# Optimization experiments

Hardware: AMD Instinct MI355X
Metric: run time of the kernel (lower is better)

The kernel has to match this reference:

```python
import jax, jax.numpy as jnp
import numpy as np

H = 64
N = 200000
E = 2000000
EPS = 1e-5


def layernorm(x, g, b):
    mu = jnp.mean(x, axis=-1, keepdims=True)
    var = jnp.var(x, axis=-1, keepdims=True)
    return (x - mu) * jax.lax.rsqrt(var + EPS) * g + b


def setup_inputs() -> dict:
    key = jax.random.key(0)
    ks = jax.random.split(key, 12)
    s = 0.02
    return {
        "z": jax.random.normal(ks[0], (N, H), dtype=jnp.float32),
        "pot_arcs": jax.random.randint(ks[1], (E, 2), 0, N + 1, dtype=jnp.int64),
        "root_w": jax.random.normal(ks[2], (H, 1), dtype=jnp.float32) * s,
        "root_b": jax.random.normal(ks[3], (H,), dtype=jnp.float32) * s,
        "lin1_w": jax.random.normal(ks[4], (H, H), dtype=jnp.float32) * s,
        "lin1_b": jax.random.normal(ks[5], (H,), dtype=jnp.float32) * s,
        "lin2_w": jax.random.normal(ks[6], (H, H), dtype=jnp.float32) * s,
        "lin2_b": jax.random.normal(ks[7], (H,), dtype=jnp.float32) * s,
        "bil_w": jax.random.normal(ks[8], (1, H, H), dtype=jnp.float32) * s,
        "bil_b": jax.random.normal(ks[9], (1,), dtype=jnp.float32) * s,
        "norm_g": jnp.ones((H,), dtype=jnp.float32),
        "norm_b": jnp.zeros((H,), dtype=jnp.float32),
    }


def reference(z, pot_arcs, root_w, root_b, lin1_w, lin1_b, lin2_w, lin2_b,
              bil_w, bil_b, norm_g, norm_b):
    # root feature: Linear(1->H) applied to ones((1,1)) => root_w[:,0] + root_b
    root_feat = (root_w[:, 0] + root_b)[None, :]           # [1, H]
    zz = jnp.concatenate([root_feat, z], axis=0)           # [N+1, H]
    zz = layernorm(zz, norm_g, norm_b)

    # edge gather (irregular access)
    h1 = zz[pot_arcs[:, 0]]                                # [E, H]
    h2 = zz[pot_arcs[:, 1]]                                # [E, H]

    # dual linear -> relu -> LayerNorm (dropout = identity in eval)
    x1 = layernorm(jax.nn.relu(h1 @ lin1_w.T + lin1_b), norm_g, norm_b)
    x2 = layernorm(jax.nn.relu(h2 @ lin2_w.T + lin2_b), norm_g, norm_b)

    # bilinear score: x1 @ W[0] @ x2 per edge, +b
    score = jnp.einsum('eh,hg,eg->e', x1, bil_w[0], x2) + bil_b[0]
    return score                                            # [E]
```

## Files before the change

kernel.cpp:

```cpp
#include <hip/hip_runtime.h>
#include <hip/hip_bf16.h>

typedef unsigned short u16;
typedef unsigned int u32;

typedef float f32x4 __attribute__((ext_vector_type(4)));
typedef short bf16x8 __attribute__((ext_vector_type(8)));

#define HDIM 64
#define EPS 1e-5f
#define XROW 68


__device__ __forceinline__ float wave_sum64(float v) {
    v += __shfl_xor(v, 1, 64);
    v += __shfl_xor(v, 2, 64);
    v += __shfl_xor(v, 4, 64);
    v += __shfl_xor(v, 8, 64);
    v += __shfl_xor(v, 16, 64);
    v += __shfl_xor(v, 32, 64);
    return v;
}

__device__ __forceinline__ float bcast(float v, int k) {
    return __int_as_float(__builtin_amdgcn_readlane(__float_as_int(v), k));
}

__device__ __forceinline__ u16 f2bf(float f) {
    u32 u = __float_as_uint(f);
    u32 r = (u + 0x7fffu + ((u >> 16) & 1u)) >> 16;
    return (u16)r;
}

__device__ __forceinline__ float bflo(u32 w) { return __uint_as_float(w << 16); }
__device__ __forceinline__ float bfhi(u32 w) { return __uint_as_float(w & 0xffff0000u); }

__global__ __launch_bounds__(256) void prep_kernel(
    const float* __restrict__ lin1_w, const float* __restrict__ lin2_w,
    const float* __restrict__ bil_w,
    u16* __restrict__ w1bf, u16* __restrict__ w2bf, u16* __restrict__ btbf)
{
    const int tid = threadIdx.x;
    for (int i = tid; i < 4096; i += 256) {
        w1bf[i] = f2bf(lin1_w[i]);
        w2bf[i] = f2bf(lin2_w[i]);
        const int g = i >> 6, h = i & 63;
        btbf[i] = f2bf(bil_w[h * 64 + g]);
    }
}

__device__ __forceinline__ bf16x8 load_afrag(const u16* Xs, int l, int m, int s) {
    const int row = 16 * m + (l & 15);
    const int k0  = 8 * (l >> 4) + 32 * s;
    union { uint2 u[2]; bf16x8 f; } c;
    c.u[0] = *(const uint2*)&Xs[row * XROW + k0];
    c.u[1] = *(const uint2*)&Xs[row * XROW + k0 + 4];
    return c.f;
}

__device__ __forceinline__ bf16x8 load_bfrag(const u16* __restrict__ W,
                                             int l, int t, int s) {
    const int n  = (l & 15) + 16 * t;
    const int k0 = 8 * (l >> 4) + 32 * s;
    return *(const bf16x8*)&W[n * 64 + k0];
}

__device__ __forceinline__ void relu_ln_acc(f32x4* acc, const float* biasv,
                                            const float* gv, const float* bvv) {
    float s[4] = {0.f,0.f,0.f,0.f}, q[4] = {0.f,0.f,0.f,0.f};
#pragma unroll
    for (int t = 0; t < 4; ++t)
#pragma unroll
        for (int j = 0; j < 4; ++j) {
            float v = fmaxf(acc[t][j] + biasv[t], 0.f);
            acc[t][j] = v;
            s[j] += v; q[j] = fmaf(v, v, q[j]);
        }
#pragma unroll
    for (int j = 0; j < 4; ++j) {
#pragma unroll
        for (int m = 1; m < 16; m <<= 1) {
            s[j] += __shfl_xor(s[j], m, 64);
            q[j] += __shfl_xor(q[j], m, 64);
        }
        const float mu = s[j] * 0.015625f;
        const float rs = rsqrtf(q[j] * 0.015625f - mu * mu + EPS);
#pragma unroll
        for (int t = 0; t < 4; ++t)
            acc[t][j] = (acc[t][j] - mu) * rs * gv[t] + bvv[t];
    }
}

__device__ __forceinline__ void acc_to_lds(u16* Xs, const f32x4* acc, int l, int m) {
    const int hcol = l & 15;
#pragma unroll
    for (int j = 0; j < 4; ++j) {
        const int row = 16 * m + (l >> 4) * 4 + j;
#pragma unroll
        for (int t = 0; t < 4; ++t)
            Xs[row * XROW + hcol + 16 * t] = f2bf(acc[t][j]);
    }
}

__device__ __forceinline__ void lds_to_global32(u16* __restrict__ T, const u16* Xs,
                                                int l, int n0, int nnodes) {
    const int row  = l >> 1;
    const int node = n0 + row;
    if (node >= nnodes) return;
    const int c0 = (l & 1) * 32;
    const u16* src = &Xs[row * XROW + c0];
    uint2 p[8];
#pragma unroll
    for (int j = 0; j < 8; ++j) p[j] = *(const uint2*)&src[4*j];
    uint4* d = (uint4*)(T + (size_t)node * HDIM + c0);
    d[0] = make_uint4(p[0].x, p[0].y, p[1].x, p[1].y);
    d[1] = make_uint4(p[2].x, p[2].y, p[3].x, p[3].y);
    d[2] = make_uint4(p[4].x, p[4].y, p[5].x, p[5].y);
    d[3] = make_uint4(p[6].x, p[6].y, p[7].x, p[7].y);
}

__global__ __launch_bounds__(256) void phase1_kernel(
    const float* __restrict__ z,
    const float* __restrict__ root_w, const float* __restrict__ root_b,
    const u16* __restrict__ w1bf, const float* __restrict__ lin1_b,
    const u16* __restrict__ w2bf, const float* __restrict__ lin2_b,
    const u16* __restrict__ btbf,
    const float* __restrict__ norm_g, const float* __restrict__ norm_b,
    u16* __restrict__ T1, u16* __restrict__ T2, int nnodes)
{
    __shared__ u16 XsAll[4][32 * XROW];

    const int tid = threadIdx.x;
    const int wid = tid >> 6;
    const int l   = tid & 63;
    u16* Xs = XsAll[wid];

    const int n0 = (blockIdx.x * 4 + wid) * 32;

    {
        const int row  = l >> 1;
        const int node = n0 + row;
        const int c0   = (l & 1) * 32;
        float r[32];
        if (node == 0) {
#pragma unroll
            for (int qq = 0; qq < 8; ++qq) {
                const float4 a = *(const float4*)&root_w[c0 + 4*qq];
                const float4 b = *(const float4*)&root_b[c0 + 4*qq];
                r[4*qq] = a.x + b.x; r[4*qq+1] = a.y + b.y;
                r[4*qq+2] = a.z + b.z; r[4*qq+3] = a.w + b.w;
            }
        } else if (node < nnodes) {
            const float4* zp = (const float4*)(z + (size_t)(node - 1) * HDIM + c0);
#pragma unroll
            for (int qq = 0; qq < 8; ++qq) {
                const float4 v = zp[qq];
                r[4*qq] = v.x; r[4*qq+1] = v.y; r[4*qq+2] = v.z; r[4*qq+3] = v.w;
            }
        } else {
#pragma unroll
            for (int k = 0; k < 32; ++k) r[k] = 0.f;
        }
        float s = 0.f, sq = 0.f;
#pragma unroll
        for (int k = 0; k < 32; ++k) { s += r[k]; sq = fmaf(r[k], r[k], sq); }
        s  += __shfl_xor(s, 1, 64);  sq += __shfl_xor(sq, 1, 64);
        const float mu = s * 0.015625f;
        const float rs = rsqrtf(sq * 0.015625f - mu * mu + EPS);
        u16* dst = &Xs[row * XROW + c0];
#pragma unroll
        for (int qq = 0; qq < 8; ++qq) {
            const float4 g4 = *(const float4*)&norm_g[c0 + 4*qq];
            const float4 b4 = *(const float4*)&norm_b[c0 + 4*qq];
            u16 t0 = f2bf((r[4*qq]   - mu) * rs * g4.x + b4.x);
            u16 t1 = f2bf((r[4*qq+1] - mu) * rs * g4.y + b4.y);
            u16 t2 = f2bf((r[4*qq+2] - mu) * rs * g4.z + b4.z);
            u16 t3 = f2bf((r[4*qq+3] - mu) * rs * g4.w + b4.w);
            uint2 pw;
            pw.x = (u32)t0 | ((u32)t1 << 16);
            pw.y = (u32)t2 | ((u32)t3 << 16);
            *(uint2*)&dst[4*qq] = pw;
        }
    }

    const int hcol = l & 15;
    float gv[4], bv[4], b1v[4], b2v[4];
#pragma unroll
    for (int t = 0; t < 4; ++t) {
        gv[t]  = norm_g[hcol + 16*t];
        bv[t]  = norm_b[hcol + 16*t];
        b1v[t] = lin1_b[hcol + 16*t];
        b2v[t] = lin2_b[hcol + 16*t];
    }

    bf16x8 a[2][2];
#pragma unroll
    for (int m = 0; m < 2; ++m) {
        a[m][0] = load_afrag(Xs, l, m, 0);
        a[m][1] = load_afrag(Xs, l, m, 1);
    }

    f32x4 acc2[2][4], acc1[2][4];
#pragma unroll
    for (int t = 0; t < 4; ++t) {
        const bf16x8 b0 = load_bfrag(w2bf, l, t, 0);
        const bf16x8 b1 = load_bfrag(w2bf, l, t, 1);
#pragma unroll
        for (int m = 0; m < 2; ++m) {
            f32x4 c = {0.f, 0.f, 0.f, 0.f};
            c = __builtin_amdgcn_mfma_f32_16x16x32_bf16(a[m][0], b0, c, 0, 0, 0);
            c = __builtin_amdgcn_mfma_f32_16x16x32_bf16(a[m][1], b1, c, 0, 0, 0);
            acc2[m][t] = c;
        }
    }
#pragma unroll
    for (int t = 0; t < 4; ++t) {
        const bf16x8 b0 = load_bfrag(w1bf, l, t, 0);
        const bf16x8 b1 = load_bfrag(w1bf, l, t, 1);
#pragma unroll
        for (int m = 0; m < 2; ++m) {
            f32x4 c = {0.f, 0.f, 0.f, 0.f};
            c = __builtin_amdgcn_mfma_f32_16x16x32_bf16(a[m][0], b0, c, 0, 0, 0);
            c = __builtin_amdgcn_mfma_f32_16x16x32_bf16(a[m][1], b1, c, 0, 0, 0);
            acc1[m][t] = c;
        }
    }

    relu_ln_acc(acc2[0], b2v, gv, bv);
    relu_ln_acc(acc2[1], b2v, gv, bv);
    acc_to_lds(Xs, acc2[0], l, 0);
    acc_to_lds(Xs, acc2[1], l, 1);
    lds_to_global32(T2, Xs, l, n0, nnodes);

    relu_ln_acc(acc1[0], b1v, gv, bv);
    relu_ln_acc(acc1[1], b1v, gv, bv);
    acc_to_lds(Xs, acc1[0], l, 0);
    acc_to_lds(Xs, acc1[1], l, 1);
#pragma unroll
    for (int m = 0; m < 2; ++m) {
        a[m][0] = load_afrag(Xs, l, m, 0);
        a[m][1] = load_afrag(Xs, l, m, 1);
    }

    f32x4 acc3[2][4];
#pragma unroll
    for (int t = 0; t < 4; ++t) {
        const bf16x8 b0 = load_bfrag(btbf, l, t, 0);
        const bf16x8 b1 = load_bfrag(btbf, l, t, 1);
#pragma unroll
        for (int m = 0; m < 2; ++m) {
            f32x4 c = {0.f, 0.f, 0.f, 0.f};
            c = __builtin_amdgcn_mfma_f32_16x16x32_bf16(a[m][0], b0, c, 0, 0, 0);
            c = __builtin_amdgcn_mfma_f32_16x16x32_bf16(a[m][1], b1, c, 0, 0, 0);
            acc3[m][t] = c;
        }
    }
    acc_to_lds(Xs, acc3[0], l, 0);
    acc_to_lds(Xs, acc3[1], l, 1);
    lds_to_global32(T1, Xs, l, n0, nnodes);
}

__device__ __forceinline__ float dot8(uint4 u, uint4 v) {
    float s = 0.f;
    s = fmaf(bflo(u.x), bflo(v.x), s); s = fmaf(bfhi(u.x), bfhi(v.x), s);
    s = fmaf(bflo(u.y), bflo(v.y), s); s = fmaf(bfhi(u.y), bfhi(v.y), s);
    s = fmaf(bflo(u.z), bflo(v.z), s); s = fmaf(bfhi(u.z), bfhi(v.z), s);
    s = fmaf(bflo(u.w), bflo(v.w), s); s = fmaf(bfhi(u.w), bfhi(v.w), s);
    return s;
}

__global__ __launch_bounds__(256) void phase2_kernel(
    const int* __restrict__ arcs,
    const u16* __restrict__ T1, const u16* __restrict__ T2,
    const float* __restrict__ bil_b,
    float* __restrict__ out, int E)
{
    const int gtid = blockIdx.x * 256 + threadIdx.x;
    const int wv = gtid >> 6;
    const int l  = gtid & 63;
    const int l8 = l & 7;
    const int le = l >> 3;
    const int e0 = wv * 16 + le;
    const int e1 = e0 + 8;
    const bool ok0 = e0 < E, ok1 = e1 < E;

    uint4 u0, v0, u1, v1;
    if (ok0) {
        const int i0 = arcs[2 * e0], j0 = arcs[2 * e0 + 1];
        u0 = *((const uint4*)(T1 + (size_t)i0 * HDIM) + l8);
        v0 = *((const uint4*)(T2 + (size_t)j0 * HDIM) + l8);
    }
    if (ok1) {
        const int i1 = arcs[2 * e1], j1 = arcs[2 * e1 + 1];
        u1 = *((const uint4*)(T1 + (size_t)i1 * HDIM) + l8);
        v1 = *((const uint4*)(T2 + (size_t)j1 * HDIM) + l8);
    }

    float s0 = ok0 ? dot8(u0, v0) : 0.f;
    float s1 = ok1 ? dot8(u1, v1) : 0.f;

    s0 += __shfl_xor(s0, 1, 64);  s1 += __shfl_xor(s1, 1, 64);
    s0 += __shfl_xor(s0, 2, 64);  s1 += __shfl_xor(s1, 2, 64);
    s0 += __shfl_xor(s0, 4, 64);  s1 += __shfl_xor(s1, 4, 64);

    if (l8 == 0) {
        const float bb = bil_b[0];
        if (ok0) __builtin_nontemporal_store(s0 + bb, &out[e0]);
        if (ok1) __builtin_nontemporal_store(s1 + bb, &out[e1]);
    }
}

__device__ __forceinline__ float lnorm_w(float v, float g, float b) {
    float mu = wave_sum64(v) * 0.015625f;
    float d  = v - mu;
    float var = wave_sum64(d * d) * 0.015625f;
    return d * rsqrtf(var + EPS) * g + b;
}

__global__ __launch_bounds__(256) void edge_direct_kernel(
    const float* __restrict__ z, const int* __restrict__ arcs,
    const float* __restrict__ root_w, const float* __restrict__ root_b,
    const float* __restrict__ lin1_w, const float* __restrict__ lin1_b,
    const float* __restrict__ lin2_w, const float* __restrict__ lin2_b,
    const float* __restrict__ bil_w, const float* __restrict__ bil_b,
    const float* __restrict__ norm_g, const float* __restrict__ norm_b,
    float* __restrict__ out, int E, int nnodes)
{
    __shared__ float W1t[4096], W2t[4096], Bs[4096];
    const int tid = threadIdx.x;
    for (int i = tid; i < 4096; i += 256) {
        int h = i >> 6, k = i & 63;
        W1t[(k << 6) | h] = lin1_w[i];
        W2t[(k << 6) | h] = lin2_w[i];
        Bs[i] = bil_w[i];
    }
    __syncthreads();

    const int lane = tid & 63;
    const float g  = norm_g[lane], bt = norm_b[lane];
    const float b1 = lin1_b[lane], b2 = lin2_b[lane];
    const float rootv = root_w[lane] + root_b[lane];

    const int gwave = (blockIdx.x * 256 + tid) >> 6;
    const int nwaves = (gridDim.x * 256) >> 6;

    for (int e = gwave; e < E; e += nwaves) {
        int i0 = arcs[2 * e], i1 = arcs[2 * e + 1];
        float v0 = (i0 == 0) ? rootv : z[(size_t)(i0 - 1) * HDIM + lane];
        float v1 = (i1 == 0) ? rootv : z[(size_t)(i1 - 1) * HDIM + lane];
        float l0 = lnorm_w(v0, g, bt);
        float l1 = lnorm_w(v1, g, bt);
        float a1 = 0.f, a2 = 0.f;
#pragma unroll
        for (int k = 0; k < 64; ++k) {
            a1 = fmaf(bcast(l0, k), W1t[(k << 6) | lane], a1);
            a2 = fmaf(bcast(l1, k), W2t[(k << 6) | lane], a2);
        }
        float x1 = lnorm_w(fmaxf(a1 + b1, 0.f), g, bt);
        float x2 = lnorm_w(fmaxf(a2 + b2, 0.f), g, bt);
        float w1 = 0.f;
#pragma unroll
        for (int h = 0; h < 64; ++h)
            w1 = fmaf(bcast(x1, h), Bs[(h << 6) | lane], w1);
        float sc = wave_sum64(w1 * x2);
        if (lane == 0) out[e] = sc + bil_b[0];
    }
}

extern "C" void kernel_launch(void* const* d_in, const int* in_sizes, int n_in,
                              void* d_out, int out_size, void* d_ws, size_t ws_size,
                              hipStream_t stream) {
    const float* z      = (const float*)d_in[0];
    const int*   arcs   = (const int*)  d_in[1];
    const float* root_w = (const float*)d_in[2];
    const float* root_b = (const float*)d_in[3];
    const float* lin1_w = (const float*)d_in[4];
    const float* lin1_b = (const float*)d_in[5];
    const float* lin2_w = (const float*)d_in[6];
    const float* lin2_b = (const float*)d_in[7];
    const float* bil_w  = (const float*)d_in[8];
    const float* bil_b  = (const float*)d_in[9];
    const float* norm_g = (const float*)d_in[10];
    const float* norm_b = (const float*)d_in[11];
    float* out = (float*)d_out;

    const int E      = in_sizes[1] / 2;
    const int nnodes = in_sizes[0] / HDIM + 1;

    const size_t tbl  = (size_t)nnodes * HDIM * sizeof(u16);
    const size_t need = 2 * tbl + 3 * 4096 * sizeof(u16);

    if (ws_size >= need) {
        u16* T1   = (u16*)d_ws;
        u16* T2   = (u16*)((char*)d_ws + tbl);
        u16* w1bf = (u16*)((char*)d_ws + 2 * tbl);
        u16* w2bf = w1bf + 4096;
        u16* btbf = w2bf + 4096;

        prep_kernel<<<1, 256, 0, stream>>>(lin1_w, lin2_w, bil_w, w1bf, w2bf, btbf);

        const int blocks1 = (nnodes + 127) / 128;
        phase1_kernel<<<blocks1, 256, 0, stream>>>(
            z, root_w, root_b, w1bf, lin1_b, w2bf, lin2_b, btbf,
            norm_g, norm_b, T1, T2, nnodes);

        const long long thr2 = (long long)E * 4;
        const int blocks2 = (int)((thr2 + 255) / 256);
        phase2_kernel<<<blocks2, 256, 0, stream>>>(arcs, T1, T2, bil_b, out, E);
    } else {
        edge_direct_kernel<<<8192, 256, 0, stream>>>(
            z, arcs, root_w, root_b, lin1_w, lin1_b, lin2_w, lin2_b,
            bil_w, bil_b, norm_g, norm_b, out, E, nnodes);
    }
}
```

Before: 132.6 us.

## Build MFMA A-fragments in registers, simplify edge gather, widen prep grid

Phase 1 now has each lane load and layer-normalize exactly the row slices it needs for its MFMA A-fragments. This skips the LDS write/read round trip, and the row statistics are reduced across lanes with shuffles. Phase 2 is rewritten to handle one edge per 8 threads instead of two edges per 8 lanes, which doubles the thread count and drops the nontemporal stores. The weight prep kernel now runs on 16 blocks instead of 1. Together these aim to cut LDS traffic and serial prep time, but phase 2 launches more threads and does less work per thread, which may hurt gather latency hiding.

```diff
diff --git a/kernel.cpp b/kernel.cpp
--- a/kernel.cpp
+++ b/kernel.cpp
@@ -32,6 +32,9 @@
     return (u16)r;
 }
 
+__device__ __forceinline__ u32 pack2(float e0, float e1) {
+    return (u32)f2bf(e0) | ((u32)f2bf(e1) << 16);
+}
 __device__ __forceinline__ float bflo(u32 w) { return __uint_as_float(w << 16); }
 __device__ __forceinline__ float bfhi(u32 w) { return __uint_as_float(w & 0xffff0000u); }
 
@@ -40,8 +43,8 @@
     const float* __restrict__ bil_w,
     u16* __restrict__ w1bf, u16* __restrict__ w2bf, u16* __restrict__ btbf)
 {
-    const int tid = threadIdx.x;
-    for (int i = tid; i < 4096; i += 256) {
+    const int gtid = blockIdx.x * 256 + threadIdx.x;
+    for (int i = gtid; i < 4096; i += gridDim.x * 256) {
         w1bf[i] = f2bf(lin1_w[i]);
         w2bf[i] = f2bf(lin2_w[i]);
         const int g = i >> 6, h = i & 63;
@@ -137,50 +140,71 @@
 
     const int n0 = (blockIdx.x * 4 + wid) * 32;
 
-    {
-        const int row  = l >> 1;
-        const int node = n0 + row;
-        const int c0   = (l & 1) * 32;
-        float r[32];
+    const int arow = l & 15;
+    const int kg   = (l >> 4) * 8;
+
+    float4 gk0 = *(const float4*)&norm_g[kg];
+    float4 gk1 = *(const float4*)&norm_g[kg + 4];
+    float4 gk2 = *(const float4*)&norm_g[kg + 32];
+    float4 gk3 = *(const float4*)&norm_g[kg + 36];
+    float4 bk0 = *(const float4*)&norm_b[kg];
+    float4 bk1 = *(const float4*)&norm_b[kg + 4];
+    float4 bk2 = *(const float4*)&norm_b[kg + 32];
+    float4 bk3 = *(const float4*)&norm_b[kg + 36];
+
+    bf16x8 a[2][2];
+#pragma unroll
+    for (int m = 0; m < 2; ++m) {
+        const int node = n0 + 16 * m + arow;
+        float r[16];
         if (node == 0) {
 #pragma unroll
-            for (int qq = 0; qq < 8; ++qq) {
-                const float4 a = *(const float4*)&root_w[c0 + 4*qq];
-                const float4 b = *(const float4*)&root_b[c0 + 4*qq];
-                r[4*qq] = a.x + b.x; r[4*qq+1] = a.y + b.y;
-                r[4*qq+2] = a.z + b.z; r[4*qq+3] = a.w + b.w;
+            for (int q = 0; q < 2; ++q) {
+                const float4 aw = *(const float4*)&root_w[kg + 4*q];
+                const float4 ab = *(const float4*)&root_b[kg + 4*q];
+                r[4*q]   = aw.x + ab.x; r[4*q+1] = aw.y + ab.y;
+                r[4*q+2] = aw.z + ab.z; r[4*q+3] = aw.w + ab.w;
+                const float4 cw = *(const float4*)&root_w[kg + 32 + 4*q];
+                const float4 cb = *(const float4*)&root_b[kg + 32 + 4*q];
+                r[8+4*q]   = cw.x + cb.x; r[8+4*q+1] = cw.y + cb.y;
+                r[8+4*q+2] = cw.z + cb.z; r[8+4*q+3] = cw.w + cb.w;
             }
         } else if (node < nnodes) {
-            const float4* zp = (const float4*)(z + (size_t)(node - 1) * HDIM + c0);
-#pragma unroll
-            for (int qq = 0; qq < 8; ++qq) {
-                const float4 v = zp[qq];
-                r[4*qq] = v.x; r[4*qq+1] = v.y; r[4*qq+2] = v.z; r[4*qq+3] = v.w;
-            }
+            const float* zp = z + (size_t)(node - 1) * HDIM + kg;
+            const float4 v0 = *(const float4*)(zp);
+            const float4 v1 = *(const float4*)(zp + 4);
+            const float4 v2 = *(const float4*)(zp + 32);
+            const float4 v3 = *(const float4*)(zp + 36);
+            r[0]=v0.x; r[1]=v0.y; r[2]=v0.z; r[3]=v0.w;
+            r[4]=v1.x; r[5]=v1.y; r[6]=v1.z; r[7]=v1.w;
+            r[8]=v2.x; r[9]=v2.y; r[10]=v2.z; r[11]=v2.w;
+            r[12]=v3.x; r[13]=v3.y; r[14]=v3.z; r[15]=v3.w;
         } else {
 #pragma unroll
-            for (int k = 0; k < 32; ++k) r[k] = 0.f;
+            for (int k = 0; k < 16; ++k) r[k] = 0.f;
         }
         float s = 0.f, sq = 0.f;
 #pragma unroll
-        for (int k = 0; k < 32; ++k) { s += r[k]; sq = fmaf(r[k], r[k], sq); }
-        s  += __shfl_xor(s, 1, 64);  sq += __shfl_xor(sq, 1, 64);
+        for (int k = 0; k < 16; ++k) { s += r[k]; sq = fmaf(r[k], r[k], sq); }
+        s += __shfl_xor(s, 16, 64);  sq += __shfl_xor(sq, 16, 64);
+        s += __shfl_xor(s, 32, 64);  sq += __shfl_xor(sq, 32, 64);
         const float mu = s * 0.015625f;
         const float rs = rsqrtf(sq * 0.015625f - mu * mu + EPS);
-        u16* dst = &Xs[row * XROW + c0];
-#pragma unroll
-        for (int qq = 0; qq < 8; ++qq) {
-            const float4 g4 = *(const float4*)&norm_g[c0 + 4*qq];
-            const float4 b4 = *(const float4*)&norm_b[c0 + 4*qq];
-            u16 t0 = f2bf((r[4*qq]   - mu) * rs * g4.x + b4.x);
-            u16 t1 = f2bf((r[4*qq+1] - mu) * rs * g4.y + b4.y);
-            u16 t2 = f2bf((r[4*qq+2] - mu) * rs * g4.z + b4.z);
-            u16 t3 = f2bf((r[4*qq+3] - mu) * rs * g4.w + b4.w);
-            uint2 pw;
-            pw.x = (u32)t0 | ((u32)t1 << 16);
-            pw.y = (u32)t2 | ((u32)t3 << 16);
-            *(uint2*)&dst[4*qq] = pw;
-        }
+
+        const float gA[8] = {gk0.x,gk0.y,gk0.z,gk0.w, gk1.x,gk1.y,gk1.z,gk1.w};
+        const float bA[8] = {bk0.x,bk0.y,bk0.z,bk0.w, bk1.x,bk1.y,bk1.z,bk1.w};
+        const float gB[8] = {gk2.x,gk2.y,gk2.z,gk2.w, gk3.x,gk3.y,gk3.z,gk3.w};
+        const float bB[8] = {bk2.x,bk2.y,bk2.z,bk2.w, bk3.x,bk3.y,bk3.z,bk3.w};
+        union { u32 u[4]; bf16x8 f; } c0, c1;
+#pragma unroll
+        for (int j = 0; j < 4; ++j) {
+            c0.u[j] = pack2((r[2*j]   - mu) * rs * gA[2*j]   + bA[2*j],
+                            (r[2*j+1] - mu) * rs * gA[2*j+1] + bA[2*j+1]);
+            c1.u[j] = pack2((r[8+2*j]   - mu) * rs * gB[2*j]   + bB[2*j],
+                            (r[8+2*j+1] - mu) * rs * gB[2*j+1] + bB[2*j+1]);
+        }
+        a[m][0] = c0.f;
+        a[m][1] = c1.f;
     }
 
     const int hcol = l & 15;
@@ -193,13 +217,6 @@
         b2v[t] = lin2_b[hcol + 16*t];
     }
 
-    bf16x8 a[2][2];
-#pragma unroll
-    for (int m = 0; m < 2; ++m) {
-        a[m][0] = load_afrag(Xs, l, m, 0);
-        a[m][1] = load_afrag(Xs, l, m, 1);
-    }
-
     f32x4 acc2[2][4], acc1[2][4];
 #pragma unroll
     for (int t = 0; t < 4; ++t) {
@@ -258,15 +275,6 @@
     acc_to_lds(Xs, acc3[0], l, 0);
     acc_to_lds(Xs, acc3[1], l, 1);
     lds_to_global32(T1, Xs, l, n0, nnodes);
-}
-
-__device__ __forceinline__ float dot8(uint4 u, uint4 v) {
-    float s = 0.f;
-    s = fmaf(bflo(u.x), bflo(v.x), s); s = fmaf(bfhi(u.x), bfhi(v.x), s);
-    s = fmaf(bflo(u.y), bflo(v.y), s); s = fmaf(bfhi(u.y), bfhi(v.y), s);
-    s = fmaf(bflo(u.z), bflo(v.z), s); s = fmaf(bfhi(u.z), bfhi(v.z), s);
-    s = fmaf(bflo(u.w), bflo(v.w), s); s = fmaf(bfhi(u.w), bfhi(v.w), s);
-    return s;
 }
 
 __global__ __launch_bounds__(256) void phase2_kernel(
@@ -275,39 +283,33 @@
     const float* __restrict__ bil_b,
     float* __restrict__ out, int E)
 {
-    const int gtid = blockIdx.x * 256 + threadIdx.x;
-    const int wv = gtid >> 6;
-    const int l  = gtid & 63;
-    const int l8 = l & 7;
-    const int le = l >> 3;
-    const int e0 = wv * 16 + le;
-    const int e1 = e0 + 8;
-    const bool ok0 = e0 < E, ok1 = e1 < E;
-
-    uint4 u0, v0, u1, v1;
-    if (ok0) {
-        const int i0 = arcs[2 * e0], j0 = arcs[2 * e0 + 1];
-        u0 = *((const uint4*)(T1 + (size_t)i0 * HDIM) + l8);
-        v0 = *((const uint4*)(T2 + (size_t)j0 * HDIM) + l8);
-    }
-    if (ok1) {
-        const int i1 = arcs[2 * e1], j1 = arcs[2 * e1 + 1];
-        u1 = *((const uint4*)(T1 + (size_t)i1 * HDIM) + l8);
-        v1 = *((const uint4*)(T2 + (size_t)j1 * HDIM) + l8);
-    }
-
-    float s0 = ok0 ? dot8(u0, v0) : 0.f;
-    float s1 = ok1 ? dot8(u1, v1) : 0.f;
-
-    s0 += __shfl_xor(s0, 1, 64);  s1 += __shfl_xor(s1, 1, 64);
-    s0 += __shfl_xor(s0, 2, 64);  s1 += __shfl_xor(s1, 2, 64);
-    s0 += __shfl_xor(s0, 4, 64);  s1 += __shfl_xor(s1, 4, 64);
-
-    if (l8 == 0) {
-        const float bb = bil_b[0];
-        if (ok0) __builtin_nontemporal_store(s0 + bb, &out[e0]);
-        if (ok1) __builtin_nontemporal_store(s1 + bb, &out[e1]);
-    }
+    const int tid = blockIdx.x * 256 + threadIdx.x;
+    const int e = tid >> 3;
+    if (e >= E) return;
+    const int l8 = tid & 7;
+
+    const int i0 = arcs[2 * e];
+    const int i1 = arcs[2 * e + 1];
+
+    const uint4* p1 = (const uint4*)(T1 + (size_t)i0 * HDIM) + l8;
+    const uint4* p2 = (const uint4*)(T2 + (size_t)i1 * HDIM) + l8;
+    uint4 u = *p1;
+    uint4 v = *p2;
+
+    float s = 0.f;
+    {
+        u32 ua[4] = {u.x, u.y, u.z, u.w};
+        u32 va[4] = {v.x, v.y, v.z, v.w};
+#pragma unroll
+        for (int i = 0; i < 4; ++i) {
+            s = fmaf(bflo(ua[i]), bflo(va[i]), s);
+            s = fmaf(bfhi(ua[i]), bfhi(va[i]), s);
+        }
+    }
+    s += __shfl_xor(s, 1, 64);
+    s += __shfl_xor(s, 2, 64);
+    s += __shfl_xor(s, 4, 64);
+    if (l8 == 0) out[e] = s + bil_b[0];
 }
 
 __device__ __forceinline__ float lnorm_w(float v, float g, float b) {
@@ -397,14 +399,14 @@
         u16* w2bf = w1bf + 4096;
         u16* btbf = w2bf + 4096;
 
-        prep_kernel<<<1, 256, 0, stream>>>(lin1_w, lin2_w, bil_w, w1bf, w2bf, btbf);
+        prep_kernel<<<16, 256, 0, stream>>>(lin1_w, lin2_w, bil_w, w1bf, w2bf, btbf);
 
         const int blocks1 = (nnodes + 127) / 128;
         phase1_kernel<<<blocks1, 256, 0, stream>>>(
             z, root_w, root_b, w1bf, lin1_b, w2bf, lin2_b, btbf,
             norm_g, norm_b, T1, T2, nnodes);
 
-        const long long thr2 = (long long)E * 4;
+        const long long thr2 = (long long)E * 8;
         const int blocks2 = (int)((thr2 + 255) / 256);
         phase2_kernel<<<blocks2, 256, 0, stream>>>(arcs, T1, T2, bil_b, out, E);
     } else {
```

After: 125.1 us. 5.7% less time.
